# Kernel tuning notes

Hardware: AMD Instinct MI355X
Metric: run time of the kernel (lower is better)

## Reference

```python
import jax, jax.numpy as jnp
import numpy as np

B, L, D = 32, 1024, 128

def setup_inputs() -> dict:
    key = jax.random.key(0)
    kq, kk, kv, ks = jax.random.split(key, 4)
    Q = jax.random.normal(kq, (B, L, D), dtype=jnp.float32)
    K = jax.random.normal(kk, (B, L, D), dtype=jnp.float32)
    V = jax.random.normal(kv, (B, L, D), dtype=jnp.float32)
    kg_sim = jax.random.uniform(ks, (B, L, L), dtype=jnp.float32)
    scale = jnp.float32(1.0 / np.sqrt(D))
    return {"Q": Q, "K": K, "V": V, "scale": scale, "kg_sim": kg_sim}

def reference(Q, K, V, scale, kg_sim):
    # attention = -1 * (Q @ K^T) * scale   [B, L, L]
    attn = -scale * jnp.einsum('bqd,bkd->bqk', Q, K)
    # attention = -softmax(attention, axis=-1)
    attn = -jax.nn.softmax(attn, axis=-1)
    # beta = softmax(attention * kg_sim, axis=-1)
    beta = jax.nn.softmax(attn * kg_sim, axis=-1)
    # context = beta @ V   [B, L, D]
    return jnp.einsum('bqk,bkd->bqd', beta, V)
```

## Files before the change

### kernel.cpp

```cpp
#include <hip/hip_runtime.h>
#include <hip/hip_bf16.h>

#define L 1024
#define D 128
#define NB 32
#define BQ 16

typedef __attribute__((ext_vector_type(8))) short short8;
typedef __attribute__((ext_vector_type(4))) short short4v;
typedef __attribute__((ext_vector_type(4))) float f32x4;

__device__ __forceinline__ unsigned short f2bf(float f) {
    union { float f; unsigned int u; } x; x.f = f;
    unsigned int r = x.u + 0x7FFF + ((x.u >> 16) & 1);
    return (unsigned short)(r >> 16);
}
__device__ __forceinline__ float bf2f(unsigned short u) {
    union { unsigned int u; float f; } x; x.u = ((unsigned int)u) << 16;
    return x.f;
}
__device__ __forceinline__ float fast_exp2(float x) {
#if __has_builtin(__builtin_amdgcn_exp2f)
    return __builtin_amdgcn_exp2f(x);
#else
    return exp2f(x);
#endif
}

__global__ void prep_kernel(const float* __restrict__ K, const float* __restrict__ V,
                            unsigned short* __restrict__ Kb, unsigned short* __restrict__ Vt) {
    __shared__ unsigned short t[32][40];
    int id = blockIdx.x;
    int tid = threadIdx.x;
    if (id < 2048) {
        size_t base = (size_t)id * 2048 + (size_t)tid * 8;
        float4 a = *(const float4*)(K + base);
        float4 c = *(const float4*)(K + base + 4);
        short8 o;
        o[0] = (short)f2bf(a.x); o[1] = (short)f2bf(a.y);
        o[2] = (short)f2bf(a.z); o[3] = (short)f2bf(a.w);
        o[4] = (short)f2bf(c.x); o[5] = (short)f2bf(c.y);
        o[6] = (short)f2bf(c.z); o[7] = (short)f2bf(c.w);
        *(short8*)(Kb + base) = o;
        return;
    }
    id -= 2048;
    int b = id >> 7;
    int rest = id & 127;
    int kt = rest >> 2, dt = rest & 3;
    int k0 = kt * 32, d0 = dt * 32;

    int kl = tid >> 3, dl4 = (tid & 7) * 4;
    const float* src = V + (((size_t)b * L + (k0 + kl)) * D) + d0 + dl4;
    float4 v = *(const float4*)src;
    t[dl4 + 0][kl] = f2bf(v.x);
    t[dl4 + 1][kl] = f2bf(v.y);
    t[dl4 + 2][kl] = f2bf(v.z);
    t[dl4 + 3][kl] = f2bf(v.w);
    __syncthreads();

    int dl = tid >> 3, kl4 = (tid & 7) * 4;
    unsigned short* dst = Vt + (((size_t)b * D + (d0 + dl)) * L) + k0 + kl4;
    short4v o;
    o[0] = (short)t[dl][kl4 + 0];
    o[1] = (short)t[dl][kl4 + 1];
    o[2] = (short)t[dl][kl4 + 2];
    o[3] = (short)t[dl][kl4 + 3];
    *(short4v*)dst = o;
}

__global__ __launch_bounds__(256, 2)
void attn_kernel(const float* __restrict__ Q, const unsigned short* __restrict__ Kb,
                 const float* __restrict__ scale_p, const float* __restrict__ kg,
                 const unsigned short* __restrict__ Vt, float* __restrict__ out) {
    __shared__ unsigned short S16[BQ * 1032];
    __shared__ float zpart[4][BQ];
    __shared__ float row_scale[BQ];
    __shared__ float dummy[16];

    const int tid = threadIdx.x;
    const int b  = blockIdx.x >> 6;
    const int q0 = (blockIdx.x & 63) * BQ;
    const float nsc = -scale_p[0] * 1.44269504f;

    const int wave = tid >> 6, lane = tid & 63;
    const int lr = lane & 15;
    const int lg = lane >> 4;
    const int row = tid >> 4, l = tid & 15;

    const float* kgrow = kg + (((size_t)b * L) + q0 + row) * L + l * 4;
    float4 kgv[16];
#pragma unroll
    for (int j = 0; j < 16; j++) kgv[j] = *(const float4*)(kgrow + 64 * j);

    short8 aq[4];
#pragma unroll
    for (int kb = 0; kb < 4; kb++) {
        const float* qp = Q + (((size_t)b * L) + q0 + lr) * D + kb * 32 + lg * 8;
        float4 v0 = *(const float4*)qp;
        float4 v1 = *(const float4*)(qp + 4);
        short8 o;
        o[0] = (short)f2bf(v0.x * nsc); o[1] = (short)f2bf(v0.y * nsc);
        o[2] = (short)f2bf(v0.z * nsc); o[3] = (short)f2bf(v0.w * nsc);
        o[4] = (short)f2bf(v1.x * nsc); o[5] = (short)f2bf(v1.y * nsc);
        o[6] = (short)f2bf(v1.z * nsc); o[7] = (short)f2bf(v1.w * nsc);
        aq[kb] = o;
    }

    f32x4 zp = {0.f, 0.f, 0.f, 0.f};
#pragma unroll 4
    for (int i = 0; i < 16; i++) {
        int ct = wave + i * 4;
        const unsigned short* kp = Kb + (((size_t)b * L) + ct * 16 + lr) * D + lg * 8;
        f32x4 acc = {0.f, 0.f, 0.f, 0.f};
#pragma unroll
        for (int kb = 0; kb < 4; kb++) {
            short8 bf = *(const short8*)(kp + kb * 32);
            acc = __builtin_amdgcn_mfma_f32_16x16x32_bf16(aq[kb], bf, acc, 0, 0, 0);
        }
#pragma unroll
        for (int r = 0; r < 4; r++) {
            float p = fast_exp2(acc[r]);
            S16[(lg * 4 + r) * 1032 + ct * 16 + lr] = f2bf(p);
            zp[r] += p;
        }
    }
#pragma unroll
    for (int m = 1; m < 16; m <<= 1) {
#pragma unroll
        for (int r = 0; r < 4; r++) zp[r] += __shfl_xor(zp[r], m, 64);
    }
    if (lr == 0) {
#pragma unroll
        for (int r = 0; r < 4; r++) zpart[wave][lg * 4 + r] = zp[r];
    }
    {
        float cs = 0.f;
#pragma unroll
        for (int j = 0; j < 16; j++) cs += kgv[j].x;
        dummy[tid & 15] = cs;
    }
    __syncthreads();

    const float iz1 = 1.0f / (zpart[0][row] + zpart[1][row] +
                              zpart[2][row] + zpart[3][row]);
    const float c1 = iz1 * 1.44269504f;
    unsigned short* srow = &S16[row * 1032];
    float z2 = 0.f;
#pragma unroll
    for (int j = 0; j < 16; j++) {
        unsigned short* p = &srow[l * 4 + 64 * j];
        short4v v = *(const short4v*)p;
        float4 g = kgv[j];
        float e0 = fast_exp2(-(bf2f((unsigned short)v[0]) * c1) * g.x);
        float e1 = fast_exp2(-(bf2f((unsigned short)v[1]) * c1) * g.y);
        float e2 = fast_exp2(-(bf2f((unsigned short)v[2]) * c1) * g.z);
        float e3 = fast_exp2(-(bf2f((unsigned short)v[3]) * c1) * g.w);
        z2 += (e0 + e1) + (e2 + e3);
        short4v o; o[0] = (short)f2bf(e0); o[1] = (short)f2bf(e1);
        o[2] = (short)f2bf(e2); o[3] = (short)f2bf(e3);
        *(short4v*)p = o;
    }
#pragma unroll
    for (int m = 1; m < 16; m <<= 1) z2 += __shfl_xor(z2, m, 64);
    if (l == 0) row_scale[row] = 1.0f / z2;
    __syncthreads();

    const int dt0 = wave * 2;
    f32x4 acc0 = {0.f, 0.f, 0.f, 0.f}, acc1 = {0.f, 0.f, 0.f, 0.f};
    const unsigned short* vt0 = Vt + (((size_t)b * D) + dt0 * 16 + lr) * L + lg * 8;
    const unsigned short* vt1 = vt0 + (size_t)16 * L;
    const unsigned short* brow = &S16[lr * 1032 + lg * 8];
#pragma unroll 8
    for (int kb = 0; kb < 32; kb++) {
        short8 a  = *(const short8*)(brow + kb * 32);
        short8 b0 = *(const short8*)(vt0 + kb * 32);
        short8 b1 = *(const short8*)(vt1 + kb * 32);
        acc0 = __builtin_amdgcn_mfma_f32_16x16x32_bf16(a, b0, acc0, 0, 0, 0);
        acc1 = __builtin_amdgcn_mfma_f32_16x16x32_bf16(a, b1, acc1, 0, 0, 0);
    }
    float* orow = out + (((size_t)b * L) + q0) * D;
#pragma unroll
    for (int r = 0; r < 4; r++) {
        int rq = lg * 4 + r;
        float rs = row_scale[rq];
        orow[(size_t)rq * D + dt0 * 16 + lr]       = acc0[r] * rs;
        orow[(size_t)rq * D + (dt0 + 1) * 16 + lr] = acc1[r] * rs;
    }
}

extern "C" void kernel_launch(void* const* d_in, const int* in_sizes, int n_in,
                              void* d_out, int out_size, void* d_ws, size_t ws_size,
                              hipStream_t stream) {
    const float* Q     = (const float*)d_in[0];
    const float* K     = (const float*)d_in[1];
    const float* V     = (const float*)d_in[2];
    const float* scale = (const float*)d_in[3];
    const float* kg    = (const float*)d_in[4];
    float* out = (float*)d_out;
    unsigned short* Vt = (unsigned short*)d_ws;
    unsigned short* Kb = (unsigned short*)d_ws + (size_t)NB * D * L;

    prep_kernel<<<6144, 256, 0, stream>>>(K, V, Kb, Vt);
    attn_kernel<<<NB * (L / BQ), 256, 0, stream>>>(Q, Kb, scale, kg, Vt, out);
}
```

Before: 338.5 us.

## Stream kg_sim through double-buffered LDS via async global_load_lds

Replaces the 16 float4 register prefetch of each kg_sim row with asynchronous global-to-LDS loads into a two-chunk ring buffer. The second softmax now runs in eight 128-column chunks, with manual vmcnt waits so later chunk loads overlap compute on earlier ones. With those registers freed, launch bounds go from 2 to 3 blocks per SM to raise occupancy. The cost is about 16 KB more LDS per block and fragile hand-written waitcnt encodings that assume each wave only reads rows it loaded itself.

```diff
diff --git a/kernel.cpp b/kernel.cpp
--- a/kernel.cpp
+++ b/kernel.cpp
@@ -5,10 +5,13 @@
 #define D 128
 #define NB 32
 #define BQ 16
+#define SS 1032
+#define KGS 130
 
 typedef __attribute__((ext_vector_type(8))) short short8;
 typedef __attribute__((ext_vector_type(4))) short short4v;
 typedef __attribute__((ext_vector_type(4))) float f32x4;
+typedef __attribute__((ext_vector_type(2))) float f32x2;
 
 __device__ __forceinline__ unsigned short f2bf(float f) {
     union { float f; unsigned int u; } x; x.f = f;
@@ -25,6 +28,11 @@
 #else
     return exp2f(x);
 #endif
+}
+__device__ __forceinline__ void dma4(const float* g, float* l) {
+    __builtin_amdgcn_global_load_lds(
+        (const __attribute__((address_space(1))) void*)(const void*)g,
+        (__attribute__((address_space(3))) void*)(void*)l, 4, 0, 0);
 }
 
 __global__ void prep_kernel(const float* __restrict__ K, const float* __restrict__ V,
@@ -69,14 +77,14 @@
     *(short4v*)dst = o;
 }
 
-__global__ __launch_bounds__(256, 2)
+__global__ __launch_bounds__(256, 3)
 void attn_kernel(const float* __restrict__ Q, const unsigned short* __restrict__ Kb,
                  const float* __restrict__ scale_p, const float* __restrict__ kg,
                  const unsigned short* __restrict__ Vt, float* __restrict__ out) {
-    __shared__ unsigned short S16[BQ * 1032];
+    __shared__ unsigned short S16[BQ * SS];
+    __shared__ float kgbuf[2][BQ * KGS];
     __shared__ float zpart[4][BQ];
     __shared__ float row_scale[BQ];
-    __shared__ float dummy[16];
 
     const int tid = threadIdx.x;
     const int b  = blockIdx.x >> 6;
@@ -84,14 +92,23 @@
     const float nsc = -scale_p[0] * 1.44269504f;
 
     const int wave = tid >> 6, lane = tid & 63;
-    const int lr = lane & 15;
-    const int lg = lane >> 4;
+    const int lr = lane & 15, lg = lane >> 4;
     const int row = tid >> 4, l = tid & 15;
 
-    const float* kgrow = kg + (((size_t)b * L) + q0 + row) * L + l * 4;
-    float4 kgv[16];
-#pragma unroll
-    for (int j = 0; j < 16; j++) kgv[j] = *(const float4*)(kgrow + 64 * j);
+    const float* kgbase = kg + ((size_t)(b * L + q0)) * L;
+
+#define ISSUE_CHUNK(c) do {                                                     \
+        _Pragma("unroll")                                                       \
+        for (int rr = 0; rr < 4; rr++) {                                        \
+            const float* s_ = kgbase + (size_t)(4 * wave + rr) * L + (c) * 128 + lane; \
+            float* d_ = &kgbuf[(c) & 1][(4 * wave + rr) * KGS];                 \
+            dma4(s_, d_);                                                       \
+            dma4(s_ + 64, d_ + 64);                                             \
+        }                                                                       \
+    } while (0)
+
+    ISSUE_CHUNK(0);
+    ISSUE_CHUNK(1);
 
     short8 aq[4];
 #pragma unroll
@@ -121,7 +138,7 @@
 #pragma unroll
         for (int r = 0; r < 4; r++) {
             float p = fast_exp2(acc[r]);
-            S16[(lg * 4 + r) * 1032 + ct * 16 + lr] = f2bf(p);
+            S16[(lg * 4 + r) * SS + ct * 16 + lr] = f2bf(p);
             zp[r] += p;
         }
     }
@@ -133,34 +150,51 @@
     if (lr == 0) {
 #pragma unroll
         for (int r = 0; r < 4; r++) zpart[wave][lg * 4 + r] = zp[r];
-    }
-    {
-        float cs = 0.f;
-#pragma unroll
-        for (int j = 0; j < 16; j++) cs += kgv[j].x;
-        dummy[tid & 15] = cs;
     }
     __syncthreads();
 
     const float iz1 = 1.0f / (zpart[0][row] + zpart[1][row] +
                               zpart[2][row] + zpart[3][row]);
     const float c1 = iz1 * 1.44269504f;
-    unsigned short* srow = &S16[row * 1032];
+    unsigned short* srow = &S16[row * SS];
     float z2 = 0.f;
-#pragma unroll
-    for (int j = 0; j < 16; j++) {
-        unsigned short* p = &srow[l * 4 + 64 * j];
-        short4v v = *(const short4v*)p;
-        float4 g = kgv[j];
-        float e0 = fast_exp2(-(bf2f((unsigned short)v[0]) * c1) * g.x);
-        float e1 = fast_exp2(-(bf2f((unsigned short)v[1]) * c1) * g.y);
-        float e2 = fast_exp2(-(bf2f((unsigned short)v[2]) * c1) * g.z);
-        float e3 = fast_exp2(-(bf2f((unsigned short)v[3]) * c1) * g.w);
-        z2 += (e0 + e1) + (e2 + e3);
-        short4v o; o[0] = (short)f2bf(e0); o[1] = (short)f2bf(e1);
-        o[2] = (short)f2bf(e2); o[3] = (short)f2bf(e3);
-        *(short4v*)p = o;
-    }
+
+    auto proc = [&](int cc) {
+        const float* gk = &kgbuf[cc & 1][row * KGS + l * 8];
+        unsigned short* p = &srow[cc * 128 + l * 8];
+        short4v v0 = *(const short4v*)p;
+        short4v v1 = *(const short4v*)(p + 4);
+        f32x2 g0 = *(const f32x2*)gk;
+        f32x2 g1 = *(const f32x2*)(gk + 2);
+        f32x2 g2 = *(const f32x2*)(gk + 4);
+        f32x2 g3 = *(const f32x2*)(gk + 6);
+        float e0 = fast_exp2(-(bf2f((unsigned short)v0[0]) * c1) * g0[0]);
+        float e1 = fast_exp2(-(bf2f((unsigned short)v0[1]) * c1) * g0[1]);
+        float e2 = fast_exp2(-(bf2f((unsigned short)v0[2]) * c1) * g1[0]);
+        float e3 = fast_exp2(-(bf2f((unsigned short)v0[3]) * c1) * g1[1]);
+        float e4 = fast_exp2(-(bf2f((unsigned short)v1[0]) * c1) * g2[0]);
+        float e5 = fast_exp2(-(bf2f((unsigned short)v1[1]) * c1) * g2[1]);
+        float e6 = fast_exp2(-(bf2f((unsigned short)v1[2]) * c1) * g3[0]);
+        float e7 = fast_exp2(-(bf2f((unsigned short)v1[3]) * c1) * g3[1]);
+        z2 += ((e0 + e1) + (e2 + e3)) + ((e4 + e5) + (e6 + e7));
+        short4v o0, o1;
+        o0[0] = (short)f2bf(e0); o0[1] = (short)f2bf(e1);
+        o0[2] = (short)f2bf(e2); o0[3] = (short)f2bf(e3);
+        o1[0] = (short)f2bf(e4); o1[1] = (short)f2bf(e5);
+        o1[2] = (short)f2bf(e6); o1[3] = (short)f2bf(e7);
+        *(short4v*)p = o0;
+        *(short4v*)(p + 4) = o1;
+    };
+
+    proc(0);  ISSUE_CHUNK(2);
+    proc(1);  ISSUE_CHUNK(3);
+    __builtin_amdgcn_s_waitcnt(0xF78); proc(2); ISSUE_CHUNK(4);
+    __builtin_amdgcn_s_waitcnt(0xF78); proc(3); ISSUE_CHUNK(5);
+    __builtin_amdgcn_s_waitcnt(0xF78); proc(4); ISSUE_CHUNK(6);
+    __builtin_amdgcn_s_waitcnt(0xF78); proc(5); ISSUE_CHUNK(7);
+    __builtin_amdgcn_s_waitcnt(0xF78); proc(6);
+    __builtin_amdgcn_s_waitcnt(0xF70); proc(7);
+
 #pragma unroll
     for (int m = 1; m < 16; m <<= 1) z2 += __shfl_xor(z2, m, 64);
     if (l == 0) row_scale[row] = 1.0f / z2;
@@ -170,7 +204,7 @@
     f32x4 acc0 = {0.f, 0.f, 0.f, 0.f}, acc1 = {0.f, 0.f, 0.f, 0.f};
     const unsigned short* vt0 = Vt + (((size_t)b * D) + dt0 * 16 + lr) * L + lg * 8;
     const unsigned short* vt1 = vt0 + (size_t)16 * L;
-    const unsigned short* brow = &S16[lr * 1032 + lg * 8];
+    const unsigned short* brow = &S16[lr * SS + lg * 8];
 #pragma unroll 8
     for (int kb = 0; kb < 32; kb++) {
         short8 a  = *(const short8*)(brow + kb * 32);
@@ -187,6 +221,7 @@
         orow[(size_t)rq * D + dt0 * 16 + lr]       = acc0[r] * rs;
         orow[(size_t)rq * D + (dt0 + 1) * 16 + lr] = acc1[r] * rs;
     }
+#undef ISSUE_CHUNK
 }
 
 extern "C" void kernel_launch(void* const* d_in, const int* in_sizes, int n_in,
```

Measured after the change: 329.1 us. -2.8%, faster.
